# Performance work log

Measured on AMD Instinct MI355X. Metric: run time of the kernel, lower is better.

## Reference

```python
import jax, jax.numpy as jnp
import numpy as np

EMBED = 1024
HEADS = 16
HEAD_DIM = EMBED // HEADS


def setup_inputs() -> dict:
    key = jax.random.key(0)
    k1, k2, k3, k4, k5 = jax.random.split(key, 5)
    B, S = 2, 2048
    scale = 1.0 / np.sqrt(EMBED)
    return {
        "input_tensor": jax.random.normal(k1, (B, S, EMBED), dtype=jnp.float32),
        "qkv_weight": jax.random.normal(k2, (3 * EMBED, EMBED), dtype=jnp.float32) * scale,
        "qkv_bias": jax.random.normal(k3, (3 * EMBED,), dtype=jnp.float32) * 0.02,
        "out_weight": jax.random.normal(k4, (EMBED, EMBED), dtype=jnp.float32) * scale,
        "out_bias": jax.random.normal(k5, (EMBED,), dtype=jnp.float32) * 0.02,
    }


def reference(input_tensor, qkv_weight, qkv_bias, out_weight, out_bias):
    B, S, D = input_tensor.shape
    # fused QKV projection: (B,S,3D)
    qkv = jnp.einsum("bsd,ed->bse", input_tensor, qkv_weight) + qkv_bias
    q, k, v = jnp.split(qkv, 3, axis=-1)
    # reshape to (B,H,S,hd)
    def to_heads(t):
        return t.reshape(B, S, HEADS, HEAD_DIM).transpose(0, 2, 1, 3)
    q, k, v = to_heads(q), to_heads(k), to_heads(v)
    scores = jnp.einsum("bhqd,bhkd->bhqk", q, k) / jnp.sqrt(jnp.float32(HEAD_DIM))
    probs = jax.nn.softmax(scores, axis=-1)  # dropout is identity in eval
    attn = jnp.einsum("bhqk,bhkd->bhqd", probs, v)
    attn = attn.transpose(0, 2, 1, 3).reshape(B, S, D)
    out = jnp.einsum("bsd,ed->bse", attn, out_weight) + out_bias
    return out
```

## Files before the change

### kernel.cpp

```cpp
#include <hip/hip_runtime.h>
#include <stdint.h>

#define EMBED 1024
#define HEADS 16
#define HD 64
#define D3 3072
#define SEQ 2048
#define MROWS 4096

typedef __attribute__((ext_vector_type(8))) short short8;
typedef __attribute__((ext_vector_type(4))) float f32x4;

static __device__ __forceinline__ ushort f2bf(float f) {
    uint32_t u = __builtin_bit_cast(uint32_t, f);
    uint32_t r = (u + 0x7fffu + ((u >> 16) & 1u)) >> 16;
    return (ushort)r;
}

static __device__ __forceinline__ void glds16(const void* g, void* l) {
    __builtin_amdgcn_global_load_lds(
        (const __attribute__((address_space(1))) uint32_t*)g,
        (__attribute__((address_space(3))) uint32_t*)(uintptr_t)l,
        16, 0, 0);
}

static __device__ __forceinline__ uint32_t cvt_pk_bf16(float lo, float hi) {
    uint32_t r;
    asm("v_cvt_pk_bf16_f32 %0, %1, %2" : "=v"(r) : "v"(lo), "v"(hi));
    return r;
}

__global__ __launch_bounds__(256) void cvt_f32_bf16(const float* __restrict__ in,
                                                    ushort* __restrict__ out, int n4) {
    int i = blockIdx.x * 256 + threadIdx.x;
    if (i < n4) {
        float4 v = reinterpret_cast<const float4*>(in)[i];
        ushort4 o = { f2bf(v.x), f2bf(v.y), f2bf(v.z), f2bf(v.w) };
        reinterpret_cast<ushort4*>(out)[i] = o;
    }
}

template<int OUT_BF16>
__global__ __launch_bounds__(256) void gemm_bt_mfma(
    const ushort* __restrict__ A, const ushort* __restrict__ W,
    const float* __restrict__ bias, void* __restrict__ Cout,
    int M, int N, int K)
{
    __shared__ __align__(16) ushort As[128 * 32];
    __shared__ __align__(16) ushort Bs[128 * 32];

    const int t = threadIdx.x;
    const int lane = t & 63;
    const int w = t >> 6;
    const int wm = w >> 1, wn = w & 1;
    const int bm = blockIdx.y * 128, bn = blockIdx.x * 128;
    const int r16 = lane & 15, g = lane >> 4;

    f32x4 acc[4][4];
#pragma unroll
    for (int i = 0; i < 4; ++i)
#pragma unroll
        for (int j = 0; j < 4; ++j) acc[i][j] = (f32x4){0.f, 0.f, 0.f, 0.f};

    for (int k0 = 0; k0 < K; k0 += 32) {
#pragma unroll
        for (int p = 0; p < 2; ++p) {
            int c = t + p * 256;
            int row = c >> 2;
            int sg = (c & 3) ^ (row & 3);
            glds16(A + (size_t)(bm + row) * K + k0 + sg * 8, (char*)As + c * 16);
            glds16(W + (size_t)(bn + row) * K + k0 + sg * 8, (char*)Bs + c * 16);
        }
        __syncthreads();

        short8 af[4], bf[4];
#pragma unroll
        for (int mt = 0; mt < 4; ++mt) {
            int row = wm * 64 + mt * 16 + r16;
            int off = (g * 16) ^ ((row & 3) << 4);
            af[mt] = *reinterpret_cast<const short8*>((const char*)As + row * 64 + off);
        }
#pragma unroll
        for (int nt = 0; nt < 4; ++nt) {
            int row = wn * 64 + nt * 16 + r16;
            int off = (g * 16) ^ ((row & 3) << 4);
            bf[nt] = *reinterpret_cast<const short8*>((const char*)Bs + row * 64 + off);
        }
#pragma unroll
        for (int mt = 0; mt < 4; ++mt)
#pragma unroll
            for (int nt = 0; nt < 4; ++nt)
                acc[mt][nt] = __builtin_amdgcn_mfma_f32_16x16x32_bf16(
                    af[mt], bf[nt], acc[mt][nt], 0, 0, 0);
        __syncthreads();
    }

#pragma unroll
    for (int mt = 0; mt < 4; ++mt) {
#pragma unroll
        for (int nt = 0; nt < 4; ++nt) {
            int col = bn + wn * 64 + nt * 16 + r16;
            float bv = bias[col];
#pragma unroll
            for (int r = 0; r < 4; ++r) {
                size_t rowg = (size_t)(bm + wm * 64 + mt * 16 + g * 4 + r);
                float v = acc[mt][nt][r] + bv;
                if (OUT_BF16) ((ushort*)Cout)[rowg * N + col] = f2bf(v);
                else          ((float*)Cout)[rowg * N + col] = v;
            }
        }
    }
}

__global__ __launch_bounds__(256) void attn_mfma(
    const ushort* __restrict__ qkv, ushort* __restrict__ outb)
{
    __shared__ __align__(16) ushort lds[20480];

    const int t = threadIdx.x, lane = t & 63, w = t >> 6;
    const int qt = blockIdx.x, bh = blockIdx.y;
    const int b = bh >> 4, h = bh & 15;
    const int r16 = lane & 15, g = lane >> 4;

    const ushort* Qb = qkv + (size_t)b * SEQ * D3 + h * HD;
    const ushort* Kb = Qb + EMBED;
    const ushort* Vb = Qb + 2 * EMBED;

    ushort* Pw = lds + 16384 + w * 1024;

    short8 qf[2];
    {
        const ushort* qrow = Qb + (size_t)(qt * 64 + w * 16 + r16) * D3 + g * 8;
#pragma unroll
        for (int ks = 0; ks < 2; ++ks)
            qf[ks] = *reinterpret_cast<const short8*>(qrow + ks * 32);
    }

    uint4 vv[2];
    auto stage_K = [&](int tile, ushort* dst) {
#pragma unroll
        for (int p = 0; p < 2; ++p) {
            int c = t + p * 256;
            int row = c >> 3;
            int sg = (c & 7) ^ (row & 7);
            glds16(Kb + (size_t)(tile * 64 + row) * D3 + sg * 8, (char*)dst + c * 16);
        }
    };
    auto load_V = [&](int tile) {
#pragma unroll
        for (int p = 0; p < 2; ++p) {
            int dseg = w * 2 + p;
            vv[p] = *reinterpret_cast<const uint4*>(
                Vb + (size_t)(tile * 64 + lane) * D3 + dseg * 8);
        }
    };
    auto write_V = [&](ushort* dst) {
#pragma unroll
        for (int p = 0; p < 2; ++p) {
            int dseg = w * 2 + p;
            ushort tmp[8];
            *reinterpret_cast<uint4*>(tmp) = vv[p];
#pragma unroll
            for (int j = 0; j < 8; ++j) {
                int d = dseg * 8 + j;
                int off = (lane * 2) ^ ((d & 7) << 4);
                *(ushort*)((char*)dst + d * 128 + off) = tmp[j];
            }
        }
    };

    f32x4 o[4];
#pragma unroll
    for (int dt = 0; dt < 4; ++dt) o[dt] = (f32x4){0.f, 0.f, 0.f, 0.f};
    float m2 = -1e30f, lsum = 0.f;

    const float SC = 0.18033688011112042f;

    stage_K(0, lds);
    load_V(0);
    write_V(lds + 8192);
    __syncthreads();

    const int NT = SEQ / 64;
    for (int kt = 0; kt < NT; ++kt) {
        const int cur = kt & 1;
        ushort* Kc = lds + cur * 4096;
        ushort* Vc = lds + 8192 + cur * 4096;
        ushort* Kn = lds + (cur ^ 1) * 4096;
        ushort* Vn = lds + 8192 + (cur ^ 1) * 4096;
        const bool more = (kt + 1 < NT);

        if (more) { stage_K(kt + 1, Kn); load_V(kt + 1); }

        f32x4 s[4];
#pragma unroll
        for (int ct = 0; ct < 4; ++ct) s[ct] = (f32x4){0.f, 0.f, 0.f, 0.f};
#pragma unroll
        for (int ct = 0; ct < 4; ++ct) {
#pragma unroll
            for (int ks = 0; ks < 2; ++ks) {
                int row = r16 + 16 * ct;
                int off = ((g + 4 * ks) * 16) ^ ((row & 7) << 4);
                short8 kf = *reinterpret_cast<const short8*>((const char*)Kc + row * 128 + off);
                s[ct] = __builtin_amdgcn_mfma_f32_16x16x32_bf16(kf, qf[ks], s[ct], 0, 0, 0);
            }
        }

        float sv[4][4];
        float pmax = -1e30f;
#pragma unroll
        for (int ct = 0; ct < 4; ++ct)
#pragma unroll
            for (int r = 0; r < 4; ++r) {
                sv[ct][r] = s[ct][r] * SC;
                pmax = fmaxf(pmax, sv[ct][r]);
            }
        pmax = fmaxf(pmax, __shfl_xor(pmax, 16));
        pmax = fmaxf(pmax, __shfl_xor(pmax, 32));

        if (!__all(pmax - m2 <= 8.0f)) {
            float mn = fmaxf(m2, pmax);
            float corr = exp2f(m2 - mn);
            lsum *= corr;
#pragma unroll
            for (int dt = 0; dt < 4; ++dt)
#pragma unroll
                for (int r = 0; r < 4; ++r) o[dt][r] *= corr;
            m2 = mn;
        }

        float pv[4][4], rs = 0.f;
#pragma unroll
        for (int ct = 0; ct < 4; ++ct)
#pragma unroll
            for (int r = 0; r < 4; ++r) {
                pv[ct][r] = exp2f(sv[ct][r] - m2);
                rs += pv[ct][r];
            }
        rs += __shfl_xor(rs, 16);
        rs += __shfl_xor(rs, 32);
        lsum += rs;

#pragma unroll
        for (int ct = 0; ct < 4; ++ct)
#pragma unroll
            for (int j = 0; j < 2; ++j) {
                uint32_t pk = cvt_pk_bf16(pv[ct][2 * j], pv[ct][2 * j + 1]);
                int off = ((16 * ct + 4 * g + 2 * j) * 2) ^ ((r16 & 7) << 4);
                *(uint32_t*)((char*)Pw + r16 * 128 + off) = pk;
            }

        asm volatile("s_waitcnt lgkmcnt(0)" ::: "memory");
        __builtin_amdgcn_sched_barrier(0);

        short8 pf[2];
#pragma unroll
        for (int ks = 0; ks < 2; ++ks) {
            int off = ((g + 4 * ks) * 16) ^ ((r16 & 7) << 4);
            pf[ks] = *reinterpret_cast<const short8*>((const char*)Pw + r16 * 128 + off);
        }
#pragma unroll
        for (int dt = 0; dt < 4; ++dt) {
#pragma unroll
            for (int ks = 0; ks < 2; ++ks) {
                int row = r16 + 16 * dt;
                int off = ((g + 4 * ks) * 16) ^ ((row & 7) << 4);
                short8 vf = *reinterpret_cast<const short8*>((const char*)Vc + row * 128 + off);
                o[dt] = __builtin_amdgcn_mfma_f32_16x16x32_bf16(vf, pf[ks], o[dt], 0, 0, 0);
            }
        }

        if (more) write_V(Vn);
        __syncthreads();
    }

    const size_t orow = (size_t)b * SEQ + qt * 64 + w * 16 + r16;
    float inv = 1.f / lsum;
#pragma unroll
    for (int dt = 0; dt < 4; ++dt) {
        ushort4 ov;
        ov.x = f2bf(o[dt][0] * inv);
        ov.y = f2bf(o[dt][1] * inv);
        ov.z = f2bf(o[dt][2] * inv);
        ov.w = f2bf(o[dt][3] * inv);
        *reinterpret_cast<ushort4*>(&outb[orow * EMBED + h * HD + dt * 16 + g * 4]) = ov;
    }
}

extern "C" void kernel_launch(void* const* d_in, const int* in_sizes, int n_in,
                              void* d_out, int out_size, void* d_ws, size_t ws_size,
                              hipStream_t stream)
{
    const float* x    = (const float*)d_in[0];
    const float* wqkv = (const float*)d_in[1];
    const float* bqkv = (const float*)d_in[2];
    const float* wo   = (const float*)d_in[3];
    const float* bo   = (const float*)d_in[4];
    float* out = (float*)d_out;

    ushort* xb    = (ushort*)d_ws;
    ushort* wqkvb = xb + (size_t)MROWS * EMBED;
    ushort* wob   = wqkvb + (size_t)D3 * EMBED;
    ushort* qkvb  = wob + (size_t)EMBED * EMBED;
    ushort* attnb = qkvb + (size_t)MROWS * D3;

    cvt_f32_bf16<<<4096, 256, 0, stream>>>(x,    xb,    MROWS * EMBED / 4);
    cvt_f32_bf16<<<3072, 256, 0, stream>>>(wqkv, wqkvb, D3 * EMBED / 4);
    cvt_f32_bf16<<<1024, 256, 0, stream>>>(wo,   wob,   EMBED * EMBED / 4);

    gemm_bt_mfma<1><<<dim3(D3 / 128, MROWS / 128), 256, 0, stream>>>(
        xb, wqkvb, bqkv, qkvb, MROWS, D3, EMBED);

    attn_mfma<<<dim3(SEQ / 64, 2 * HEADS), 256, 0, stream>>>(qkvb, attnb);

    gemm_bt_mfma<0><<<dim3(EMBED / 128, MROWS / 128), 256, 0, stream>>>(
        attnb, wob, bo, out, MROWS, EMBED, EMBED);
}
```

Before: 234.8 us.

## Switch attention to 32x32x16 MFMA with 128-query tiles per block

The attention kernel now uses 32x32x16 bf16 MFMA instead of 16x16x32, with each wave owning 32 query rows, so a block covers 128 queries and the grid halves. This doubles reuse of each staged K/V tile per block and cuts K/V global traffic and staging per query. It also raises wave priority around the MFMA sections and fuses exp, bf16 packing and LDS store of P into one loop. The grid shrinks to 512 blocks, which may lower occupancy balance, and register pressure rises with the larger accumulators.

```diff
diff --git a/kernel.cpp b/kernel.cpp
--- a/kernel.cpp
+++ b/kernel.cpp
@@ -10,6 +10,7 @@
 
 typedef __attribute__((ext_vector_type(8))) short short8;
 typedef __attribute__((ext_vector_type(4))) float f32x4;
+typedef __attribute__((ext_vector_type(16))) float f32x16;
 
 static __device__ __forceinline__ ushort f2bf(float f) {
     uint32_t u = __builtin_bit_cast(uint32_t, f);
@@ -115,25 +116,25 @@
 __global__ __launch_bounds__(256) void attn_mfma(
     const ushort* __restrict__ qkv, ushort* __restrict__ outb)
 {
-    __shared__ __align__(16) ushort lds[20480];
+    __shared__ __align__(16) ushort lds[24576];
 
     const int t = threadIdx.x, lane = t & 63, w = t >> 6;
     const int qt = blockIdx.x, bh = blockIdx.y;
     const int b = bh >> 4, h = bh & 15;
-    const int r16 = lane & 15, g = lane >> 4;
+    const int q31 = lane & 31, hi = lane >> 5;
 
     const ushort* Qb = qkv + (size_t)b * SEQ * D3 + h * HD;
     const ushort* Kb = Qb + EMBED;
     const ushort* Vb = Qb + 2 * EMBED;
 
-    ushort* Pw = lds + 16384 + w * 1024;
-
-    short8 qf[2];
+    ushort* Pw = lds + 16384 + w * 2048;
+
+    short8 qf[4];
     {
-        const ushort* qrow = Qb + (size_t)(qt * 64 + w * 16 + r16) * D3 + g * 8;
-#pragma unroll
-        for (int ks = 0; ks < 2; ++ks)
-            qf[ks] = *reinterpret_cast<const short8*>(qrow + ks * 32);
+        const ushort* qrow = Qb + (size_t)(qt * 128 + w * 32 + q31) * D3 + 8 * hi;
+#pragma unroll
+        for (int ks = 0; ks < 4; ++ks)
+            qf[ks] = *reinterpret_cast<const short8*>(qrow + ks * 16);
     }
 
     uint4 vv[2];
@@ -169,9 +170,11 @@
         }
     };
 
-    f32x4 o[4];
-#pragma unroll
-    for (int dt = 0; dt < 4; ++dt) o[dt] = (f32x4){0.f, 0.f, 0.f, 0.f};
+    f32x16 o[2];
+#pragma unroll
+    for (int db = 0; db < 2; ++db)
+#pragma unroll
+        for (int r = 0; r < 16; ++r) o[db][r] = 0.f;
     float m2 = -1e30f, lsum = 0.f;
 
     const float SC = 0.18033688011112042f;
@@ -192,30 +195,34 @@
 
         if (more) { stage_K(kt + 1, Kn); load_V(kt + 1); }
 
-        f32x4 s[4];
-#pragma unroll
-        for (int ct = 0; ct < 4; ++ct) s[ct] = (f32x4){0.f, 0.f, 0.f, 0.f};
-#pragma unroll
-        for (int ct = 0; ct < 4; ++ct) {
-#pragma unroll
-            for (int ks = 0; ks < 2; ++ks) {
-                int row = r16 + 16 * ct;
-                int off = ((g + 4 * ks) * 16) ^ ((row & 7) << 4);
+        f32x16 s[2];
+#pragma unroll
+        for (int cb = 0; cb < 2; ++cb)
+#pragma unroll
+            for (int r = 0; r < 16; ++r) s[cb][r] = 0.f;
+
+        __builtin_amdgcn_s_setprio(1);
+#pragma unroll
+        for (int cb = 0; cb < 2; ++cb) {
+            int row = cb * 32 + q31;
+            int swz = (row & 7) << 4;
+#pragma unroll
+            for (int ks = 0; ks < 4; ++ks) {
+                int off = (32 * ks + 16 * hi) ^ swz;
                 short8 kf = *reinterpret_cast<const short8*>((const char*)Kc + row * 128 + off);
-                s[ct] = __builtin_amdgcn_mfma_f32_16x16x32_bf16(kf, qf[ks], s[ct], 0, 0, 0);
-            }
-        }
-
-        float sv[4][4];
+                s[cb] = __builtin_amdgcn_mfma_f32_32x32x16_bf16(kf, qf[ks], s[cb], 0, 0, 0);
+            }
+        }
+        __builtin_amdgcn_s_setprio(0);
+
         float pmax = -1e30f;
 #pragma unroll
-        for (int ct = 0; ct < 4; ++ct)
-#pragma unroll
-            for (int r = 0; r < 4; ++r) {
-                sv[ct][r] = s[ct][r] * SC;
-                pmax = fmaxf(pmax, sv[ct][r]);
-            }
-        pmax = fmaxf(pmax, __shfl_xor(pmax, 16));
+        for (int cb = 0; cb < 2; ++cb)
+#pragma unroll
+            for (int r = 0; r < 16; ++r) {
+                s[cb][r] *= SC;
+                pmax = fmaxf(pmax, s[cb][r]);
+            }
         pmax = fmaxf(pmax, __shfl_xor(pmax, 32));
 
         if (!__all(pmax - m2 <= 8.0f)) {
@@ -223,67 +230,70 @@
             float corr = exp2f(m2 - mn);
             lsum *= corr;
 #pragma unroll
-            for (int dt = 0; dt < 4; ++dt)
-#pragma unroll
-                for (int r = 0; r < 4; ++r) o[dt][r] *= corr;
+            for (int db = 0; db < 2; ++db)
+#pragma unroll
+                for (int r = 0; r < 16; ++r) o[db][r] *= corr;
             m2 = mn;
         }
 
-        float pv[4][4], rs = 0.f;
-#pragma unroll
-        for (int ct = 0; ct < 4; ++ct)
-#pragma unroll
-            for (int r = 0; r < 4; ++r) {
-                pv[ct][r] = exp2f(sv[ct][r] - m2);
-                rs += pv[ct][r];
-            }
-        rs += __shfl_xor(rs, 16);
+        float rs = 0.f;
+        int pswz = (q31 & 7) << 4;
+#pragma unroll
+        for (int cb = 0; cb < 2; ++cb)
+#pragma unroll
+            for (int r = 0; r < 16; r += 2) {
+                float p0 = exp2f(s[cb][r] - m2);
+                float p1 = exp2f(s[cb][r + 1] - m2);
+                rs += p0 + p1;
+                uint32_t pk = cvt_pk_bf16(p0, p1);
+                int kc = 32 * cb + (r & 3) + 8 * (r >> 2) + 4 * hi;
+                int off = (kc * 2) ^ pswz;
+                *(uint32_t*)((char*)Pw + q31 * 128 + off) = pk;
+            }
         rs += __shfl_xor(rs, 32);
         lsum += rs;
 
-#pragma unroll
-        for (int ct = 0; ct < 4; ++ct)
-#pragma unroll
-            for (int j = 0; j < 2; ++j) {
-                uint32_t pk = cvt_pk_bf16(pv[ct][2 * j], pv[ct][2 * j + 1]);
-                int off = ((16 * ct + 4 * g + 2 * j) * 2) ^ ((r16 & 7) << 4);
-                *(uint32_t*)((char*)Pw + r16 * 128 + off) = pk;
-            }
-
         asm volatile("s_waitcnt lgkmcnt(0)" ::: "memory");
         __builtin_amdgcn_sched_barrier(0);
 
-        short8 pf[2];
-#pragma unroll
-        for (int ks = 0; ks < 2; ++ks) {
-            int off = ((g + 4 * ks) * 16) ^ ((r16 & 7) << 4);
-            pf[ks] = *reinterpret_cast<const short8*>((const char*)Pw + r16 * 128 + off);
-        }
-#pragma unroll
-        for (int dt = 0; dt < 4; ++dt) {
-#pragma unroll
-            for (int ks = 0; ks < 2; ++ks) {
-                int row = r16 + 16 * dt;
-                int off = ((g + 4 * ks) * 16) ^ ((row & 7) << 4);
+        short8 pB[4];
+#pragma unroll
+        for (int ks = 0; ks < 4; ++ks) {
+            int off = (32 * ks + 16 * hi) ^ pswz;
+            pB[ks] = *reinterpret_cast<const short8*>((const char*)Pw + q31 * 128 + off);
+        }
+        __builtin_amdgcn_s_setprio(1);
+#pragma unroll
+        for (int db = 0; db < 2; ++db) {
+            int row = db * 32 + q31;
+            int swz = (row & 7) << 4;
+#pragma unroll
+            for (int ks = 0; ks < 4; ++ks) {
+                int off = (32 * ks + 16 * hi) ^ swz;
                 short8 vf = *reinterpret_cast<const short8*>((const char*)Vc + row * 128 + off);
-                o[dt] = __builtin_amdgcn_mfma_f32_16x16x32_bf16(vf, pf[ks], o[dt], 0, 0, 0);
-            }
-        }
+                o[db] = __builtin_amdgcn_mfma_f32_32x32x16_bf16(vf, pB[ks], o[db], 0, 0, 0);
+            }
+        }
+        __builtin_amdgcn_s_setprio(0);
 
         if (more) write_V(Vn);
         __syncthreads();
     }
 
-    const size_t orow = (size_t)b * SEQ + qt * 64 + w * 16 + r16;
+    const size_t orow = (size_t)b * SEQ + qt * 128 + w * 32 + q31;
     float inv = 1.f / lsum;
 #pragma unroll
-    for (int dt = 0; dt < 4; ++dt) {
-        ushort4 ov;
-        ov.x = f2bf(o[dt][0] * inv);
-        ov.y = f2bf(o[dt][1] * inv);
-        ov.z = f2bf(o[dt][2] * inv);
-        ov.w = f2bf(o[dt][3] * inv);
-        *reinterpret_cast<ushort4*>(&outb[orow * EMBED + h * HD + dt * 16 + g * 4]) = ov;
+    for (int db = 0; db < 2; ++db) {
+#pragma unroll
+        for (int m = 0; m < 4; ++m) {
+            int d0 = 32 * db + 8 * m + 4 * hi;
+            ushort4 ov;
+            ov.x = f2bf(o[db][4 * m + 0] * inv);
+            ov.y = f2bf(o[db][4 * m + 1] * inv);
+            ov.z = f2bf(o[db][4 * m + 2] * inv);
+            ov.w = f2bf(o[db][4 * m + 3] * inv);
+            *reinterpret_cast<ushort4*>(&outb[orow * EMBED + h * HD + d0]) = ov;
+        }
     }
 }
 
@@ -311,7 +321,7 @@
     gemm_bt_mfma<1><<<dim3(D3 / 128, MROWS / 128), 256, 0, stream>>>(
         xb, wqkvb, bqkv, qkvb, MROWS, D3, EMBED);
 
-    attn_mfma<<<dim3(SEQ / 64, 2 * HEADS), 256, 0, stream>>>(qkvb, attnb);
+    attn_mfma<<<dim3(SEQ / 128, 2 * HEADS), 256, 0, stream>>>(qkvb, attnb);
 
     gemm_bt_mfma<0><<<dim3(EMBED / 128, MROWS / 128), 256, 0, stream>>>(
         attnb, wob, bo, out, MROWS, EMBED, EMBED);
```

New measurement: 224.5 us. 4.4% less time.
